# Optimization experiments

Measured on AMD Instinct MI355X. Metric: run time of the kernel, lower is better.

## Reference

```python
import jax, jax.numpy as jnp
import numpy as np

# pywt coif5 dec_lo (30 taps)
COIF5_DEC_LO = np.array([
    -9.517657273819165e-08, -1.6744288576823017e-07, 2.0637618513646814e-06,
    3.7346551751414047e-06, -2.1315026809955787e-05, -4.134043227251251e-05,
    0.00014054114970203437, 0.00030225958181306315, -0.0006381313430451114,
    -0.0016628637020130838, 0.0024333732126576722, 0.006764185448053083,
    -0.009164231162481846, -0.01976177894257264, 0.03268357426711183,
    0.0412892087501817, -0.10557420870333893, -0.06203596396290357,
    0.4379916261718371, 0.7742896036529562, 0.4215662066908515,
    -0.05204316317624377, -0.09192001055969624, 0.02816802897093635,
    0.023408156785839195, -0.010131117519849788, -0.004159358781386048,
    0.0021782363581090178, 0.00035858968789573785, -0.00021208083980379827,
], dtype=np.float32)


def _hilbert(x):
    # scipy.fftpack.hilbert: y_j = 1j*sign(j)*X_j, DC and Nyquist zeroed
    n = x.size
    X = np.fft.fft(x)
    sign = np.zeros(n)
    sign[1:(n + 1) // 2] = 1.0
    sign[n // 2 + 1:] = -1.0
    return np.real(np.fft.ifft(X * 1j * sign)).astype(np.float32)


def _make_filters():
    gl = COIF5_DEC_LO
    L = gl.size
    # QMF: dec_hi[k] = (-1)^(k+1) * dec_lo[L-1-k]
    gh = (((-1.0) ** (np.arange(L) + 1)) * gl[::-1]).astype(np.float32)
    fl = _hilbert(gl)
    fh = _hilbert(gh)
    return (jnp.asarray(gl), jnp.asarray(gh), jnp.asarray(fl), jnp.asarray(fh))


# torch bicubic (a=-0.75), scale 0.5, align_corners=False: src = 2*i + 0.5,
# fractional offset is always 0.5 -> fixed 4-tap stride-2 stencil.
_W0, _W1, _W2, _W3 = -0.09375, 0.59375, 0.59375, -0.09375


def _down2_last(x):
    # downsample last axis by 2 with edge-clamped borders (matches torch clamp)
    n = x.shape[-1]
    pad = [(0, 0)] * (x.ndim - 1) + [(1, 1)]
    xp = jnp.pad(x, pad, mode='edge')
    base = 2 * jnp.arange(n // 2)  # tap positions in padded coords
    return (_W0 * xp[..., base] + _W1 * xp[..., base + 1]
            + _W2 * xp[..., base + 2] + _W3 * xp[..., base + 3])


def _downsample(x):
    x = _down2_last(x)                                        # W axis
    x = jnp.swapaxes(_down2_last(jnp.swapaxes(x, -1, -2)), -1, -2)  # H axis
    return x


def _qwt(image, gl, gh, fl, fh):
    # In the source, _column/_row_convolve never shift X per tap and the
    # centered crop exactly removes the reflect padding, so
    # colfilter(X, h) == rowfilter(X, h) == X * sum(h)  (exact).
    filt = lambda x, h: x * jnp.sum(h)

    gl_d = _downsample(filt(image, gl))
    gh_d = _downsample(filt(image, gh))
    fl_d = _downsample(filt(image, fl))
    fh_d = _downsample(filt(image, fh))

    lglg = filt(gl_d, gl); lghg = filt(gl_d, gh); lglf = filt(gl_d, fl); lghf = filt(gl_d, fh)
    hglg = filt(gh_d, gl); hghg = filt(gh_d, gh); hglf = filt(gh_d, fl); hghf = filt(gh_d, fh)
    lflg = filt(fl_d, gl); lfhg = filt(fl_d, gh); lflf = filt(fl_d, fl); lfhf = filt(fl_d, fh)
    hflg = filt(fh_d, gl); hfhg = filt(fh_d, gh); hflf = filt(fh_d, fl); hfhf = filt(fh_d, fh)

    return (jnp.concatenate((lglg, lflg, lglf, lflf), axis=1),
            jnp.concatenate((lghg, lfhg, lghf, lfhf), axis=1),
            jnp.concatenate((hglg, hflg, hglf, hflf), axis=1),
            jnp.concatenate((hghg, hfhg, hghf, hfhf), axis=1))


def setup_inputs() -> dict:
    key = jax.random.key(0)
    image = jax.random.normal(key, (16, 3, 512, 512), dtype=jnp.float32)
    gl, gh, fl, fh = _make_filters()
    return {"image": image, "gl": gl, "gh": gh, "fl": fl, "fh": fh}


def reference(image, gl, gh, fl, fh):
    return _qwt(image, gl, gh, fl, fh)
```

## Files before the change

### kernel.cpp

```cpp
#include <hip/hip_runtime.h>


#define BW0 -0.09375f
#define BW1  0.59375f
#define BW2  0.59375f
#define BW3 -0.09375f

#define H_IN  512
#define W_IN  512
#define H_OUT 256
#define W_OUT 256
#define PLANE_OUT (H_OUT * W_OUT)
#define TENSOR_STRIDE (16 * 12 * PLANE_OUT)

typedef __attribute__((ext_vector_type(4))) float f32x4;

__global__ __launch_bounds__(256) void qwt_fused_kernel(
    const float* __restrict__ img,
    const float* __restrict__ gl, const float* __restrict__ gh,
    const float* __restrict__ fl, const float* __restrict__ fh,
    float* __restrict__ out)
{
    __shared__ float s_scale[16];
    __shared__ __align__(16) float sD[16][W_OUT];

    const int tid = threadIdx.x;

    if (tid < 64) {
        float vgl = 0.f, vgh = 0.f, vfl = 0.f, vfh = 0.f;
        if (tid < 30) { vgl = gl[tid]; vgh = gh[tid]; vfl = fl[tid]; vfh = fh[tid]; }
        #pragma unroll
        for (int m = 32; m >= 1; m >>= 1) {
            vgl += __shfl_xor(vgl, m);
            vgh += __shfl_xor(vgh, m);
            vfl += __shfl_xor(vfl, m);
            vfh += __shfl_xor(vfh, m);
        }
        if (tid < 16) {
            const int t = tid >> 2, cb = tid & 3;
            const float A = (t < 2) ? ((cb & 1) ? vfl : vgl)
                                    : ((cb & 1) ? vfh : vgh);
            const float B = (t & 1) ? ((cb < 2) ? vgh : vfh)
                                    : ((cb < 2) ? vgl : vfl);
            s_scale[tid] = A * B;
        }
    }

    const int blk = blockIdx.x;
    const int s   = blk & 15;
    const int bc  = blk >> 4;

    const float* plane = img + (size_t)bc * (H_IN * W_IN);

    const int w4  = tid & 63;
    const int hpL = tid >> 6;

    const int cbase = w4 * 8;
    int clo = cbase - 1; if (clo < 0) clo = 0;
    int chi = cbase + 8; if (chi > W_IN - 1) chi = W_IN - 1;

    #pragma unroll
    for (int u = 0; u < 2; ++u) {
        const int hp = hpL + 4 * u;

        int r[6];
        #pragma unroll
        for (int i = 0; i < 6; ++i) {
            int rr = 32 * s + 4 * hp - 1 + i;
            r[i] = rr < 0 ? 0 : (rr > H_IN - 1 ? H_IN - 1 : rr);
        }

        float hv[6][4];
        #pragma unroll
        for (int i = 0; i < 6; ++i) {
            const float* rowp = plane + (size_t)r[i] * W_IN;
            const float4 a  = *(const float4*)(rowp + cbase);
            const float4 b4 = *(const float4*)(rowp + cbase + 4);
            const float v0 = rowp[clo];
            const float v9 = rowp[chi];
            const float v1 = a.x,  v2 = a.y,  v3 = a.z,  v4 = a.w;
            const float v5 = b4.x, v6 = b4.y, v7 = b4.z, v8 = b4.w;
            hv[i][0] = BW0 * v0 + BW1 * v1 + BW2 * v2 + BW3 * v3;
            hv[i][1] = BW0 * v2 + BW1 * v3 + BW2 * v4 + BW3 * v5;
            hv[i][2] = BW0 * v4 + BW1 * v5 + BW2 * v6 + BW3 * v7;
            hv[i][3] = BW0 * v6 + BW1 * v7 + BW2 * v8 + BW3 * v9;
        }

        f32x4 d0, d1;
        d0.x = BW0 * hv[0][0] + BW1 * hv[1][0] + BW2 * hv[2][0] + BW3 * hv[3][0];
        d0.y = BW0 * hv[0][1] + BW1 * hv[1][1] + BW2 * hv[2][1] + BW3 * hv[3][1];
        d0.z = BW0 * hv[0][2] + BW1 * hv[1][2] + BW2 * hv[2][2] + BW3 * hv[3][2];
        d0.w = BW0 * hv[0][3] + BW1 * hv[1][3] + BW2 * hv[2][3] + BW3 * hv[3][3];
        d1.x = BW0 * hv[2][0] + BW1 * hv[3][0] + BW2 * hv[4][0] + BW3 * hv[5][0];
        d1.y = BW0 * hv[2][1] + BW1 * hv[3][1] + BW2 * hv[4][1] + BW3 * hv[5][1];
        d1.z = BW0 * hv[2][2] + BW1 * hv[3][2] + BW2 * hv[4][2] + BW3 * hv[5][2];
        d1.w = BW0 * hv[2][3] + BW1 * hv[3][3] + BW2 * hv[4][3] + BW3 * hv[5][3];

        *(f32x4*)&sD[2 * hp    ][4 * w4] = d0;
        *(f32x4*)&sD[2 * hp + 1][4 * w4] = d1;
    }

    __syncthreads();

    const int wave = tid >> 6;
    const int lane = tid & 63;
    const int c  = bc % 3;
    const int b  = bc / 3;

    float* outT = out + (size_t)wave * TENSOR_STRIDE
                + (size_t)b * (12 * PLANE_OUT)
                + (size_t)c * PLANE_OUT
                + (size_t)(16 * s) * W_OUT
                + (size_t)(4 * lane);

    #pragma unroll
    for (int cb = 0; cb < 4; ++cb) {
        const float sc = s_scale[wave * 4 + cb];
        float* p = outT + (size_t)cb * (3 * PLANE_OUT);
        #pragma unroll
        for (int rr = 0; rr < 16; ++rr) {
            f32x4 v = *(const f32x4*)&sD[rr][4 * lane];
            f32x4 o;
            o.x = v.x * sc; o.y = v.y * sc; o.z = v.z * sc; o.w = v.w * sc;
            __builtin_nontemporal_store(o, (f32x4*)(p + (size_t)rr * W_OUT));
        }
    }
}

extern "C" void kernel_launch(void* const* d_in, const int* in_sizes, int n_in,
                              void* d_out, int out_size, void* d_ws, size_t ws_size,
                              hipStream_t stream) {
    const float* img = (const float*)d_in[0];
    const float* gl  = (const float*)d_in[1];
    const float* gh  = (const float*)d_in[2];
    const float* fl  = (const float*)d_in[3];
    const float* fh  = (const float*)d_in[4];
    float* out = (float*)d_out;

    const int threads = 256;
    const int blocks  = 48 * 16;
    qwt_fused_kernel<<<blocks, threads, 0, stream>>>(img, gl, gh, fl, fh, out);
}
```

Measured before the change: 246.4 us.

## Split fused kernel into downsample pass and XCD-aware scatter pass via workspace

Replaces the single fused kernel with two launches. The first writes the downsampled planes to a workspace buffer. The second uses 6144 blocks to read that buffer, scale it, and write each of the 16 output slots, mapping blocks so each XCD handles a fixed set of planes. The aim is more parallelism and better L2 locality for the write-dominated output phase. In exchange it adds a workspace round trip (about 12 MB written and read back) and a second launch. The old fused kernel stays as a fallback when no workspace is available.

```diff
diff --git a/kernel.cpp b/kernel.cpp
--- a/kernel.cpp
+++ b/kernel.cpp
@@ -15,45 +15,18 @@
 
 typedef __attribute__((ext_vector_type(4))) float f32x4;
 
-__global__ __launch_bounds__(256) void qwt_fused_kernel(
-    const float* __restrict__ img,
-    const float* __restrict__ gl, const float* __restrict__ gh,
-    const float* __restrict__ fl, const float* __restrict__ fh,
-    float* __restrict__ out)
+__global__ __launch_bounds__(256) void qwt_downsample_kernel(
+    const float* __restrict__ img, float* __restrict__ wsD)
 {
-    __shared__ float s_scale[16];
-    __shared__ __align__(16) float sD[16][W_OUT];
-
+    const int blk = blockIdx.x;
+    const int bc  = blk % 48;
+    const int s   = blk / 48;
     const int tid = threadIdx.x;
-
-    if (tid < 64) {
-        float vgl = 0.f, vgh = 0.f, vfl = 0.f, vfh = 0.f;
-        if (tid < 30) { vgl = gl[tid]; vgh = gh[tid]; vfl = fl[tid]; vfh = fh[tid]; }
-        #pragma unroll
-        for (int m = 32; m >= 1; m >>= 1) {
-            vgl += __shfl_xor(vgl, m);
-            vgh += __shfl_xor(vgh, m);
-            vfl += __shfl_xor(vfl, m);
-            vfh += __shfl_xor(vfh, m);
-        }
-        if (tid < 16) {
-            const int t = tid >> 2, cb = tid & 3;
-            const float A = (t < 2) ? ((cb & 1) ? vfl : vgl)
-                                    : ((cb & 1) ? vfh : vgh);
-            const float B = (t & 1) ? ((cb < 2) ? vgh : vfh)
-                                    : ((cb < 2) ? vgl : vfl);
-            s_scale[tid] = A * B;
-        }
-    }
-
-    const int blk = blockIdx.x;
-    const int s   = blk & 15;
-    const int bc  = blk >> 4;
-
-    const float* plane = img + (size_t)bc * (H_IN * W_IN);
-
     const int w4  = tid & 63;
     const int hpL = tid >> 6;
+
+    const float* plane  = img + (size_t)bc * (H_IN * W_IN);
+    float*       dplane = wsD + (size_t)bc * PLANE_OUT;
 
     const int cbase = w4 * 8;
     int clo = cbase - 1; if (clo < 0) clo = 0;
@@ -96,6 +69,151 @@
         d1.z = BW0 * hv[2][2] + BW1 * hv[3][2] + BW2 * hv[4][2] + BW3 * hv[5][2];
         d1.w = BW0 * hv[2][3] + BW1 * hv[3][3] + BW2 * hv[4][3] + BW3 * hv[5][3];
 
+        const int row = 16 * s + 2 * hp;
+        *(f32x4*)(dplane + (size_t)row       * W_OUT + 4 * w4) = d0;
+        *(f32x4*)(dplane + (size_t)(row + 1) * W_OUT + 4 * w4) = d1;
+    }
+}
+
+__global__ __launch_bounds__(256) void qwt_scatter_kernel(
+    const float* __restrict__ wsD,
+    const float* __restrict__ gl, const float* __restrict__ gh,
+    const float* __restrict__ fl, const float* __restrict__ fh,
+    float* __restrict__ out)
+{
+    __shared__ float s_scale[16];
+    const int tid = threadIdx.x;
+
+    if (tid < 64) {
+        float vgl = 0.f, vgh = 0.f, vfl = 0.f, vfh = 0.f;
+        if (tid < 30) { vgl = gl[tid]; vgh = gh[tid]; vfl = fl[tid]; vfh = fh[tid]; }
+        #pragma unroll
+        for (int m = 32; m >= 1; m >>= 1) {
+            vgl += __shfl_xor(vgl, m);
+            vgh += __shfl_xor(vgh, m);
+            vfl += __shfl_xor(vfl, m);
+            vfh += __shfl_xor(vfh, m);
+        }
+        if (tid < 16) {
+            const int t = tid >> 2, cb = tid & 3;
+            const float A = (t < 2) ? ((cb & 1) ? vfl : vgl)
+                                    : ((cb & 1) ? vfh : vgh);
+            const float B = (t & 1) ? ((cb < 2) ? vgh : vfh)
+                                    : ((cb < 2) ? vgl : vfl);
+            s_scale[tid] = A * B;
+        }
+    }
+    __syncthreads();
+
+    const int blk  = blockIdx.x;
+    const int xcd  = blk & 7;
+    const int j    = blk >> 3;
+    const int slab = j & 7;
+    const int cb   = (j >> 3) & 3;
+    const int t    = (j >> 5) & 3;
+    const int bcg  = j >> 7;
+    const int bc   = bcg * 8 + xcd;
+    const int b    = bc / 3;
+    const int c    = bc % 3;
+
+    const float sc = s_scale[t * 4 + cb];
+
+    const float* dsrc = wsD + (size_t)bc * PLANE_OUT + (size_t)slab * 32 * W_OUT;
+    float* dst = out + (size_t)t * TENSOR_STRIDE
+               + (size_t)b  * (12 * PLANE_OUT)
+               + (size_t)cb * (3 * PLANE_OUT)
+               + (size_t)c  * PLANE_OUT
+               + (size_t)slab * 32 * W_OUT;
+
+    const int tf = tid * 4;
+    #pragma unroll
+    for (int sw = 0; sw < 8; ++sw) {
+        const int off = sw * 1024 + tf;
+        f32x4 v = *(const f32x4*)(dsrc + off);
+        f32x4 o;
+        o.x = v.x * sc; o.y = v.y * sc; o.z = v.z * sc; o.w = v.w * sc;
+        __builtin_nontemporal_store(o, (f32x4*)(dst + off));
+    }
+}
+
+__global__ __launch_bounds__(256) void qwt_fused_kernel(
+    const float* __restrict__ img,
+    const float* __restrict__ gl, const float* __restrict__ gh,
+    const float* __restrict__ fl, const float* __restrict__ fh,
+    float* __restrict__ out)
+{
+    __shared__ float s_scale[16];
+    __shared__ __align__(16) float sD[16][W_OUT];
+
+    const int tid = threadIdx.x;
+
+    if (tid < 64) {
+        float vgl = 0.f, vgh = 0.f, vfl = 0.f, vfh = 0.f;
+        if (tid < 30) { vgl = gl[tid]; vgh = gh[tid]; vfl = fl[tid]; vfh = fh[tid]; }
+        #pragma unroll
+        for (int m = 32; m >= 1; m >>= 1) {
+            vgl += __shfl_xor(vgl, m);
+            vgh += __shfl_xor(vgh, m);
+            vfl += __shfl_xor(vfl, m);
+            vfh += __shfl_xor(vfh, m);
+        }
+        if (tid < 16) {
+            const int t = tid >> 2, cb = tid & 3;
+            const float A = (t < 2) ? ((cb & 1) ? vfl : vgl)
+                                    : ((cb & 1) ? vfh : vgh);
+            const float B = (t & 1) ? ((cb < 2) ? vgh : vfh)
+                                    : ((cb < 2) ? vgl : vfl);
+            s_scale[tid] = A * B;
+        }
+    }
+
+    const int blk = blockIdx.x;
+    const int s   = blk & 15;
+    const int bc  = blk >> 4;
+
+    const float* plane = img + (size_t)bc * (H_IN * W_IN);
+
+    const int w4  = tid & 63;
+    const int hpL = tid >> 6;
+
+    const int cbase = w4 * 8;
+    int clo = cbase - 1; if (clo < 0) clo = 0;
+    int chi = cbase + 8; if (chi > W_IN - 1) chi = W_IN - 1;
+
+    #pragma unroll
+    for (int u = 0; u < 2; ++u) {
+        const int hp = hpL + 4 * u;
+        int r[6];
+        #pragma unroll
+        for (int i = 0; i < 6; ++i) {
+            int rr = 32 * s + 4 * hp - 1 + i;
+            r[i] = rr < 0 ? 0 : (rr > H_IN - 1 ? H_IN - 1 : rr);
+        }
+        float hv[6][4];
+        #pragma unroll
+        for (int i = 0; i < 6; ++i) {
+            const float* rowp = plane + (size_t)r[i] * W_IN;
+            const float4 a  = *(const float4*)(rowp + cbase);
+            const float4 b4 = *(const float4*)(rowp + cbase + 4);
+            const float v0 = rowp[clo];
+            const float v9 = rowp[chi];
+            const float v1 = a.x,  v2 = a.y,  v3 = a.z,  v4 = a.w;
+            const float v5 = b4.x, v6 = b4.y, v7 = b4.z, v8 = b4.w;
+            hv[i][0] = BW0 * v0 + BW1 * v1 + BW2 * v2 + BW3 * v3;
+            hv[i][1] = BW0 * v2 + BW1 * v3 + BW2 * v4 + BW3 * v5;
+            hv[i][2] = BW0 * v4 + BW1 * v5 + BW2 * v6 + BW3 * v7;
+            hv[i][3] = BW0 * v6 + BW1 * v7 + BW2 * v8 + BW3 * v9;
+        }
+        f32x4 d0, d1;
+        d0.x = BW0 * hv[0][0] + BW1 * hv[1][0] + BW2 * hv[2][0] + BW3 * hv[3][0];
+        d0.y = BW0 * hv[0][1] + BW1 * hv[1][1] + BW2 * hv[2][1] + BW3 * hv[3][1];
+        d0.z = BW0 * hv[0][2] + BW1 * hv[1][2] + BW2 * hv[2][2] + BW3 * hv[3][2];
+        d0.w = BW0 * hv[0][3] + BW1 * hv[1][3] + BW2 * hv[2][3] + BW3 * hv[3][3];
+        d1.x = BW0 * hv[2][0] + BW1 * hv[3][0] + BW2 * hv[4][0] + BW3 * hv[5][0];
+        d1.y = BW0 * hv[2][1] + BW1 * hv[3][1] + BW2 * hv[4][1] + BW3 * hv[5][1];
+        d1.z = BW0 * hv[2][2] + BW1 * hv[3][2] + BW2 * hv[4][2] + BW3 * hv[5][2];
+        d1.w = BW0 * hv[2][3] + BW1 * hv[3][3] + BW2 * hv[4][3] + BW3 * hv[5][3];
+
         *(f32x4*)&sD[2 * hp    ][4 * w4] = d0;
         *(f32x4*)&sD[2 * hp + 1][4 * w4] = d1;
     }
@@ -115,13 +233,13 @@
 
     #pragma unroll
     for (int cb = 0; cb < 4; ++cb) {
-        const float sc = s_scale[wave * 4 + cb];
+        const float scv = s_scale[wave * 4 + cb];
         float* p = outT + (size_t)cb * (3 * PLANE_OUT);
         #pragma unroll
         for (int rr = 0; rr < 16; ++rr) {
             f32x4 v = *(const f32x4*)&sD[rr][4 * lane];
             f32x4 o;
-            o.x = v.x * sc; o.y = v.y * sc; o.z = v.z * sc; o.w = v.w * sc;
+            o.x = v.x * scv; o.y = v.y * scv; o.z = v.z * scv; o.w = v.w * scv;
             __builtin_nontemporal_store(o, (f32x4*)(p + (size_t)rr * W_OUT));
         }
     }
@@ -137,7 +255,12 @@
     const float* fh  = (const float*)d_in[4];
     float* out = (float*)d_out;
 
-    const int threads = 256;
-    const int blocks  = 48 * 16;
-    qwt_fused_kernel<<<blocks, threads, 0, stream>>>(img, gl, gh, fl, fh, out);
-}
+    const size_t needD = (size_t)48 * PLANE_OUT * sizeof(float);
+    if (d_ws != nullptr && ws_size >= needD) {
+        float* wsD = (float*)d_ws;
+        qwt_downsample_kernel<<<768, 256, 0, stream>>>(img, wsD);
+        qwt_scatter_kernel<<<6144, 256, 0, stream>>>(wsD, gl, gh, fl, fh, out);
+    } else {
+        qwt_fused_kernel<<<768, 256, 0, stream>>>(img, gl, gh, fl, fh, out);
+    }
+}
```

Result: no change. 245.8 us (-0.2%).
